# Optimization experiments

Measured on AMD Instinct MI355X. Metric: run time of the kernel, lower is better.

Reference implementation:

```python
import jax, jax.numpy as jnp
import numpy as np

B, T, D, H = 8, 2048, 1024, 1024

def setup_inputs() -> dict:
    key = jax.random.key(0)
    k1, k2, k3, k4 = jax.random.split(key, 4)
    scale = 1.0 / np.sqrt(D)
    return {
        "x": jax.random.normal(k1, (B, T, D), dtype=jnp.float32),
        "Wq": jax.random.normal(k2, (D, H), dtype=jnp.float32) * scale,
        "Wk": jax.random.normal(k3, (D, H), dtype=jnp.float32) * scale,
        "Wv": jax.random.normal(k4, (D, H), dtype=jnp.float32) * scale,
    }

def reference(x, Wq, Wk, Wv):
    # Single-head causal self-attention (dropout in eval mode = identity)
    q = jnp.einsum('btd,dh->bth', x, Wq)
    k = jnp.einsum('btd,dh->bth', x, Wk)
    v = jnp.einsum('btd,dh->bth', x, Wv)
    inv_sqrt_h = 1.0 / jnp.sqrt(jnp.asarray(q.shape[-1], q.dtype))
    scores = jnp.einsum('bqh,bkh->bqk', q, k) * inv_sqrt_h  # [B, T, T]
    Tq = scores.shape[-1]
    causal = jnp.tril(jnp.ones((Tq, Tq), dtype=bool))
    scores = jnp.where(causal, scores, jnp.asarray(-jnp.inf, scores.dtype))
    weights = jax.nn.softmax(scores, axis=-1)
    return jnp.einsum('bqk,bkh->bqh', weights, v)
```

## Files before the change

### kernel.cpp

```cpp
#include <hip/hip_runtime.h>

#define Bn 8
#define Tn 2048
#define Dn 1024
#define Hn 1024
#define Mn (Bn * Tn)

typedef __attribute__((ext_vector_type(8))) short bf16x8;
typedef __attribute__((ext_vector_type(4))) short short4v;
typedef __attribute__((ext_vector_type(16))) float f32x16;
typedef __attribute__((ext_vector_type(4))) float f32x4;

__device__ __forceinline__ unsigned short f2bf(float f) {
  union { float f; unsigned int u; } v; v.f = f;
  unsigned int u = v.u;
  u += 0x7FFFu + ((u >> 16) & 1u);
  return (unsigned short)(u >> 16);
}
__device__ __forceinline__ float bf2f(unsigned short h) {
  union { unsigned int u; float f; } v; v.u = ((unsigned int)h) << 16;
  return v.f;
}

__device__ __forceinline__ void gload_lds16(const unsigned short* g, unsigned short* l) {
  __builtin_amdgcn_global_load_lds((const __attribute__((address_space(1))) void*)g,
                                   (__attribute__((address_space(3))) void*)l, 16, 0, 0);
}


__device__ __forceinline__ void stage128x32s(const unsigned short* gbase, size_t row_stride,
                                             unsigned short* lds, int wave, int lane) {
#pragma unroll
  for (int c = 0; c < 2; ++c) {
    int rl = c * 16 + (lane >> 2);
    int pos = (lane & 3) ^ (rl & 3) ^ ((rl >> 2) & 3);
    const unsigned short* g = gbase + (size_t)(wave * 32 + rl) * row_stride + pos * 8;
    gload_lds16(g, lds + (wave * 32 + c * 16) * 32);
  }
}
__device__ __forceinline__ void stage128x64s(const unsigned short* gbase, size_t row_stride,
                                             unsigned short* lds0, unsigned short* lds1,
                                             int wave, int lane) {
  stage128x32s(gbase, row_stride, lds0, wave, lane);
  stage128x32s(gbase + 32, row_stride, lds1, wave, lane);
}

__device__ __forceinline__ void stage256x32s(const unsigned short* gbase, size_t row_stride,
                                             unsigned short* lds, int wave, int lane) {
#pragma unroll
  for (int c = 0; c < 2; ++c) {
    int rl = c * 16 + (lane >> 2);
    int pos = (lane & 3) ^ (rl & 3) ^ ((rl >> 2) & 3);
    const unsigned short* g = gbase + (size_t)(wave * 32 + rl) * row_stride + pos * 8;
    gload_lds16(g, lds + (wave * 32 + c * 16) * 32);
  }
}

__device__ __forceinline__ void mma_bk32(const unsigned short* lA, const unsigned short* lB,
                                         int wr, int wc, int l32, int half,
                                         f32x16 acc[2][2]) {
#pragma unroll
  for (int kk = 0; kk < 2; ++kk) {
    const int pos = (kk * 2 + half) ^ (l32 & 3) ^ ((l32 >> 2) & 3);
    bf16x8 af[2], bfr[2];
#pragma unroll
    for (int m = 0; m < 2; ++m)
      af[m] = *(const bf16x8*)&lA[(wr + m * 32 + l32) * 32 + pos * 8];
#pragma unroll
    for (int n = 0; n < 2; ++n)
      bfr[n] = *(const bf16x8*)&lB[(wc + n * 32 + l32) * 32 + pos * 8];
#pragma unroll
    for (int m = 0; m < 2; ++m)
#pragma unroll
      for (int n = 0; n < 2; ++n)
        acc[m][n] = __builtin_amdgcn_mfma_f32_32x32x16_bf16(af[m], bfr[n], acc[m][n], 0, 0, 0);
  }
}

__device__ __forceinline__ void rd4(const unsigned short* p, int rbase, int rl15, int csw,
                                    bf16x8 fr[4]) {
#pragma unroll
  for (int m = 0; m < 4; ++m)
    fr[m] = *(const bf16x8*)&p[(rbase + m * 16 + rl15) * 32 + csw * 8];
}

#define QKV_BAR  __builtin_amdgcn_s_barrier()
#define QKV_LGKM asm volatile("s_waitcnt lgkmcnt(0)" ::: "memory")
#define QKV_VM8  asm volatile("s_waitcnt vmcnt(8)" ::: "memory")
#define QKV_VM4  asm volatile("s_waitcnt vmcnt(4)" ::: "memory")
#define QKV_VM0  asm volatile("s_waitcnt vmcnt(0)" ::: "memory")

__global__ __launch_bounds__(256) void k_convert(const float* __restrict__ in,
                                                 unsigned short* __restrict__ out, int n4) {
  int idx = blockIdx.x * 256 + threadIdx.x;
  if (idx >= n4) return;
  float4 v = ((const float4*)in)[idx];
  short4v o;
  o.x = (short)f2bf(v.x); o.y = (short)f2bf(v.y);
  o.z = (short)f2bf(v.z); o.w = (short)f2bf(v.w);
  *(short4v*)(out + (size_t)idx * 4) = o;
}

__global__ __launch_bounds__(256) void k_cvt_w_t(const float* __restrict__ W0,
                                                 const float* __restrict__ W1,
                                                 const float* __restrict__ W2,
                                                 unsigned short* __restrict__ Wt3) {
  const int n0 = blockIdx.x * 64, k0 = blockIdx.y * 64, w = blockIdx.z;
  const float* W = (w == 0) ? W0 : (w == 1) ? W1 : W2;
  unsigned short* Wt = Wt3 + (size_t)w * Hn * Dn;
  __shared__ unsigned short lT[64 * 65];
  const int tid = threadIdx.x;
#pragma unroll
  for (int p = 0; p < 2; ++p) {
    int o = tid + p * 256;
    int r = o >> 3, c = (o & 7) * 8;
    const float* src = W + (size_t)(k0 + r) * Hn + n0 + c;
    float4 v0 = *(const float4*)src;
    float4 v1 = *(const float4*)(src + 4);
    unsigned short* d = &lT[r * 65 + c];
    d[0] = f2bf(v0.x); d[1] = f2bf(v0.y); d[2] = f2bf(v0.z); d[3] = f2bf(v0.w);
    d[4] = f2bf(v1.x); d[5] = f2bf(v1.y); d[6] = f2bf(v1.z); d[7] = f2bf(v1.w);
  }
  __syncthreads();
#pragma unroll
  for (int p = 0; p < 2; ++p) {
    int o = tid + p * 256;
    int r2 = o >> 3, c2 = (o & 7) * 8;
    bf16x8 v;
#pragma unroll
    for (int s = 0; s < 8; ++s) v[s] = (short)lT[(c2 + s) * 65 + r2];
    *(bf16x8*)(Wt + (size_t)(n0 + r2) * Dn + k0 + c2) = v;
  }
}

__global__ __launch_bounds__(512, 2) void gemm_qkv(const unsigned short* __restrict__ A,
                                                   const unsigned short* __restrict__ Wt3,
                                                   unsigned short* __restrict__ Q,
                                                   unsigned short* __restrict__ Kb,
                                                   unsigned short* __restrict__ Vt) {
  const int f = blockIdx.x;
  const int c = f & 7;
  const int q = f >> 3;
  const int nn = q % 12;
  const int w = nn >> 2;
  const int n0 = (nn & 3) * 256;
  const int m0 = ((q / 12) * 8 + c) * 256;
  const unsigned short* Bw = Wt3 + (size_t)w * Hn * Dn;
  __shared__ unsigned short lds[2][4][256 * 32];
  const int tid = threadIdx.x;
  const int lane = tid & 63, wave = tid >> 6;
  const int wr = (wave >> 2) * 128;
  const int wc = (wave & 3) * 64;
  const int rl15 = lane & 15, l4 = lane >> 4;
  const int csw = (l4 ^ (lane & 3) ^ ((lane >> 2) & 3)) & 3;

  f32x4 acc[8][4];
#pragma unroll
  for (int m = 0; m < 8; ++m)
#pragma unroll
    for (int n = 0; n < 4; ++n) acc[m][n] = (f32x4)(0.f);

  const unsigned short* Ab = A + (size_t)m0 * Dn;
  const unsigned short* Bb = Bw + (size_t)n0 * Dn;

  unsigned short* L0AL = &lds[0][0][0];
  unsigned short* L0AH = &lds[0][1][0];
  unsigned short* L0BL = &lds[0][2][0];
  unsigned short* L0BH = &lds[0][3][0];
  unsigned short* L1AL = &lds[1][0][0];
  unsigned short* L1AH = &lds[1][1][0];
  unsigned short* L1BL = &lds[1][2][0];
  unsigned short* L1BH = &lds[1][3][0];

  bf16x8 a0[4], a1[4], b0[4];
  auto RP = [&](const unsigned short* pa, const unsigned short* pb) {
    rd4(pa, wr, rl15, csw, a0);
    rd4(pa, wr + 64, rl15, csw, a1);
    rd4(pb, wc, rl15, csw, b0);
  };
  auto M32 = [&]() {
    __builtin_amdgcn_s_setprio(1);
#pragma unroll
    for (int m = 0; m < 4; ++m)
#pragma unroll
      for (int n = 0; n < 4; ++n)
        acc[m][n] = __builtin_amdgcn_mfma_f32_16x16x32_bf16(a0[m], b0[n], acc[m][n], 0, 0, 0);
#pragma unroll
    for (int m = 0; m < 4; ++m)
#pragma unroll
      for (int n = 0; n < 4; ++n)
        acc[m + 4][n] = __builtin_amdgcn_mfma_f32_16x16x32_bf16(a1[m], b0[n], acc[m + 4][n], 0, 0, 0);
    __builtin_amdgcn_s_setprio(0);
  };

  stage256x32s(Ab +  0, Dn, L0AL, wave, lane);
  stage256x32s(Bb +  0, Dn, L0BL, wave, lane);
  stage256x32s(Ab + 32, Dn, L0AH, wave, lane);
  stage256x32s(Bb + 32, Dn, L0BH, wave, lane);
  stage256x32s(Ab + 64, Dn, L1AL, wave, lane);
  stage256x32s(Bb + 64, Dn, L1BL, wave, lane);
  QKV_VM8;
  QKV_BAR;

#pragma unroll 1
  for (int i = 0; i < 6; ++i) {
    const int s1 = 2 * i + 1, s2 = 2 * i + 2, s3 = 2 * i + 3;
    RP(L0AL, L0BL);
    stage256x32s(Ab + s1 * 64 + 32, Dn, L1AH, wave, lane);
    stage256x32s(Bb + s1 * 64 + 32, Dn, L1BH, wave, lane);
    QKV_VM8; QKV_BAR; QKV_LGKM; M32(); QKV_BAR;
    RP(L0AH, L0BH);
    stage256x32s(Ab + s2 * 64, Dn, L0AL, wave, lane);
    stage256x32s(Bb + s2 * 64, Dn, L0BL, wave, lane);
    QKV_VM8; QKV_BAR; QKV_LGKM; M32(); QKV_BAR;
    RP(L1AL, L1BL);
    stage256x32s(Ab + s2 * 64 + 32, Dn, L0AH, wave, lane);
    stage256x32s(Bb + s2 * 64 + 32, Dn, L0BH, wave, lane);
    QKV_VM8; QKV_BAR; QKV_LGKM; M32(); QKV_BAR;
    RP(L1AH, L1BH);
    stage256x32s(Ab + s3 * 64, Dn, L1AL, wave, lane);
    stage256x32s(Bb + s3 * 64, Dn, L1BL, wave, lane);
    QKV_VM8; QKV_BAR; QKV_LGKM; M32(); QKV_BAR;
  }
  RP(L0AL, L0BL);
  stage256x32s(Ab + 13 * 64 + 32, Dn, L1AH, wave, lane);
  stage256x32s(Bb + 13 * 64 + 32, Dn, L1BH, wave, lane);
  QKV_VM8; QKV_BAR; QKV_LGKM; M32(); QKV_BAR;
  RP(L0AH, L0BH);
  stage256x32s(Ab + 14 * 64, Dn, L0AL, wave, lane);
  stage256x32s(Bb + 14 * 64, Dn, L0BL, wave, lane);
  QKV_VM8; QKV_BAR; QKV_LGKM; M32(); QKV_BAR;
  RP(L1AL, L1BL);
  stage256x32s(Ab + 14 * 64 + 32, Dn, L0AH, wave, lane);
  stage256x32s(Bb + 14 * 64 + 32, Dn, L0BH, wave, lane);
  QKV_VM8; QKV_BAR; QKV_LGKM; M32(); QKV_BAR;
  RP(L1AH, L1BH);
  stage256x32s(Ab + 15 * 64, Dn, L1AL, wave, lane);
  stage256x32s(Bb + 15 * 64, Dn, L1BL, wave, lane);
  QKV_VM8; QKV_BAR; QKV_LGKM; M32(); QKV_BAR;
  RP(L0AL, L0BL);
  stage256x32s(Ab + 15 * 64 + 32, Dn, L1AH, wave, lane);
  stage256x32s(Bb + 15 * 64 + 32, Dn, L1BH, wave, lane);
  QKV_VM8; QKV_BAR; QKV_LGKM; M32(); QKV_BAR;
  RP(L0AH, L0BH);
  QKV_VM4; QKV_BAR; QKV_LGKM; M32(); QKV_BAR;
  RP(L1AL, L1BL);
  QKV_VM0; QKV_BAR; QKV_LGKM; M32(); QKV_BAR;
  RP(L1AH, L1BH);
  QKV_LGKM; M32();

  if (w != 2) {
    unsigned short* Cp = (w == 0) ? Q : Kb;
#pragma unroll
    for (int m = 0; m < 8; ++m) {
      const int row = m0 + wr + m * 16 + l4 * 4;
#pragma unroll
      for (int n = 0; n < 4; ++n) {
        const int col = n0 + wc + n * 16 + rl15;
#pragma unroll
        for (int r = 0; r < 4; ++r)
          Cp[(size_t)(row + r) * Hn + col] = f2bf(acc[m][n][r]);
      }
    }
  } else {
    const int bb = m0 >> 11;
    const int tb = m0 & 2047;
#pragma unroll
    for (int m = 0; m < 8; ++m) {
      const int t0 = tb + wr + m * 16 + l4 * 4;
#pragma unroll
      for (int n = 0; n < 4; ++n) {
        const int h = n0 + wc + n * 16 + rl15;
        short4v o;
        o.x = (short)f2bf(acc[m][n][0]);
        o.y = (short)f2bf(acc[m][n][1]);
        o.z = (short)f2bf(acc[m][n][2]);
        o.w = (short)f2bf(acc[m][n][3]);
        *(short4v*)(Vt + ((size_t)bb * Hn + h) * Tn + t0) = o;
      }
    }
  }
}

__global__ __launch_bounds__(256) void gemm_scores(const unsigned short* __restrict__ Q,
                                                   const unsigned short* __restrict__ K,
                                                   unsigned short* __restrict__ S) {
  const int f = blockIdx.x;
  const int b = f & 7;
  const int q = f >> 3;
  const int rt = 15 - (q & 15);
  const int ct = q >> 4;
  if (ct > rt) return;
  const int j0 = ct * 128, i0 = rt * 128;
  const unsigned short* Qb = Q + (size_t)b * Tn * Hn;
  const unsigned short* Kp = K + (size_t)b * Tn * Hn;
  unsigned short* Sb = S + (size_t)b * Tn * Tn;
  __shared__ unsigned short lA[2][128 * 32];
  __shared__ unsigned short lB[2][128 * 32];
  const int tid = threadIdx.x;
  const int lane = tid & 63, wave = tid >> 6;
  const int wr = (wave >> 1) * 64, wc = (wave & 1) * 64;
  const int l32 = lane & 31, half = lane >> 5;

  f32x16 acc[2][2];
#pragma unroll
  for (int m = 0; m < 2; ++m)
#pragma unroll
    for (int n = 0; n < 2; ++n) acc[m][n] = (f32x16)(0.f);

  for (int kt = 0; kt < Hn / 64; ++kt) {
    stage128x64s(Qb + (size_t)i0 * Hn + kt * 64, Hn, lA[0], lA[1], wave, lane);
    stage128x64s(Kp + (size_t)j0 * Hn + kt * 64, Hn, lB[0], lB[1], wave, lane);
    __syncthreads();
    mma_bk32(lA[0], lB[0], wr, wc, l32, half, acc);
    mma_bk32(lA[1], lB[1], wr, wc, l32, half, acc);
    __syncthreads();
  }
#pragma unroll
  for (int m = 0; m < 2; ++m)
#pragma unroll
    for (int n = 0; n < 2; ++n) {
      int col = j0 + wc + n * 32 + l32;
#pragma unroll
      for (int qd = 0; qd < 4; ++qd) {
        int rb = i0 + wr + m * 32 + 8 * qd + 4 * half;
#pragma unroll
        for (int rr = 0; rr < 4; ++rr) {
          int row = rb + rr;
          float e = (col <= row) ? __expf(acc[m][n][qd * 4 + rr] * 0.03125f) : 0.f;
          Sb[(size_t)row * Tn + col] = f2bf(e);
        }
      }
    }
}

__global__ __launch_bounds__(256) void k_rowsum(const unsigned short* __restrict__ S,
                                                float* __restrict__ l) {
  const int b = blockIdx.y;
  const int i = blockIdx.x * 4 + (threadIdx.x >> 6);
  const int lane = threadIdx.x & 63;
  const unsigned short* row = S + ((size_t)b * Tn + i) * (size_t)Tn;
  const int npad = ((i >> 7) + 1) << 7;
  float s = 0.f;
  for (int j0 = 0; j0 < npad; j0 += 512) {
    int j = j0 + lane * 8;
    if (j < npad) {
      bf16x8 v = *(const bf16x8*)(row + j);
#pragma unroll
      for (int t = 0; t < 8; ++t) s += bf2f((unsigned short)v[t]);
    }
  }
#pragma unroll
  for (int off = 32; off > 0; off >>= 1) s += __shfl_down(s, off);
  if (lane == 0) l[(size_t)b * Tn + i] = s;
}

__global__ __launch_bounds__(256) void gemm_out(const unsigned short* __restrict__ P,
                                                const unsigned short* __restrict__ Vt,
                                                const float* __restrict__ lbuf,
                                                float* __restrict__ O) {
  const int f = blockIdx.x;
  const int b = f & 7;
  const int q = f >> 3;
  const int n0 = (q & 7) * 128;
  const int rt = 15 - (q >> 3);
  const int i0 = rt * 128;
  const int nkt = (rt + 1) * 2;
  const unsigned short* Pb = P + (size_t)b * Tn * Tn;
  const unsigned short* Vb = Vt + (size_t)b * Tn * Hn;
  __shared__ unsigned short lA[2][128 * 32];
  __shared__ unsigned short lB[2][128 * 32];
  const int tid = threadIdx.x;
  const int lane = tid & 63, wave = tid >> 6;
  const int wr = (wave >> 1) * 64, wc = (wave & 1) * 64;
  const int l32 = lane & 31, half = lane >> 5;

  f32x16 acc[2][2];
#pragma unroll
  for (int m = 0; m < 2; ++m)
#pragma unroll
    for (int n = 0; n < 2; ++n) acc[m][n] = (f32x16)(0.f);

  for (int kt = 0; kt < nkt; ++kt) {
    stage128x64s(Pb + (size_t)i0 * Tn + kt * 64, Tn, lA[0], lA[1], wave, lane);
    stage128x64s(Vb + (size_t)n0 * Tn + kt * 64, Tn, lB[0], lB[1], wave, lane);
    __syncthreads();
    mma_bk32(lA[0], lB[0], wr, wc, l32, half, acc);
    mma_bk32(lA[1], lB[1], wr, wc, l32, half, acc);
    __syncthreads();
  }
#pragma unroll
  for (int m = 0; m < 2; ++m)
#pragma unroll
    for (int n = 0; n < 2; ++n) {
      int col = n0 + wc + n * 32 + l32;
#pragma unroll
      for (int qd = 0; qd < 4; ++qd) {
        int rb = i0 + wr + m * 32 + 8 * qd + 4 * half;
        float4 lv = *(const float4*)&lbuf[(size_t)b * Tn + rb];
#pragma unroll
        for (int rr = 0; rr < 4; ++rr) {
          float inv = 1.f / ((&lv.x)[rr]);
          O[((size_t)b * Tn + rb + rr) * Hn + col] = acc[m][n][qd * 4 + rr] * inv;
        }
      }
    }
}

extern "C" void kernel_launch(void* const* d_in, const int* in_sizes, int n_in,
                              void* d_out, int out_size, void* d_ws, size_t ws_size,
                              hipStream_t stream) {
  const float* x  = (const float*)d_in[0];
  const float* Wq = (const float*)d_in[1];
  const float* Wk = (const float*)d_in[2];
  const float* Wv = (const float*)d_in[3];
  float* out = (float*)d_out;

  char* ws = (char*)d_ws;
  const size_t MiB = 1024 * 1024;
  unsigned short* Wt3 = (unsigned short*)(ws + 0 * MiB);
  unsigned short* xb  = (unsigned short*)(ws + 6 * MiB);
  unsigned short* Qb  = (unsigned short*)(ws + 38 * MiB);
  unsigned short* Kb  = (unsigned short*)(ws + 70 * MiB);
  unsigned short* Vt  = (unsigned short*)(ws + 102 * MiB);
  unsigned short* S   = (unsigned short*)(ws + 134 * MiB);
  float*          lrow = (float*)(ws + 6 * MiB);

  {
    int n4 = (Mn * Dn) / 4;
    k_convert<<<dim3(n4 / 256), 256, 0, stream>>>(x, xb, n4);
  }
  {
    dim3 g(Hn / 64, Dn / 64, 3);
    k_cvt_w_t<<<g, 256, 0, stream>>>(Wq, Wk, Wv, Wt3);
  }
  {
    gemm_qkv<<<dim3(768), 512, 0, stream>>>(xb, Wt3, Qb, Kb, Vt);
  }
  {
    gemm_scores<<<dim3(2048), 256, 0, stream>>>(Qb, Kb, S);
  }
  {
    k_rowsum<<<dim3(Tn / 4, Bn), 256, 0, stream>>>(S, lrow);
  }
  {
    gemm_out<<<dim3(1024), 256, 0, stream>>>(S, Vt, lrow, out);
  }
}
```

Before: 348.1 us.

## Pipeline attention GEMMs with 16x16 MFMA, triangular grid, fused rowsum via atomics

Rewrites the scores and output GEMMs to use a double-buffered LDS pipeline with 16x16x32 MFMA, async prefetch of the next k-slices, and raised wave priority around the MFMA blocks. The scores grid now covers only the 136 lower-triangular tiles per batch instead of launching 256 and exiting early. The row-sum kernel is removed: row sums are accumulated in the scores epilogue through shuffle reductions and atomicAdd into a buffer zeroed by a memset. This cuts a separate pass over S and one launch, at the cost of atomics and more registers per thread.

```diff
diff --git a/kernel.cpp b/kernel.cpp
--- a/kernel.cpp
+++ b/kernel.cpp
@@ -8,7 +8,6 @@
 
 typedef __attribute__((ext_vector_type(8))) short bf16x8;
 typedef __attribute__((ext_vector_type(4))) short short4v;
-typedef __attribute__((ext_vector_type(16))) float f32x16;
 typedef __attribute__((ext_vector_type(4))) float f32x4;
 
 __device__ __forceinline__ unsigned short f2bf(float f) {
@@ -38,12 +37,6 @@
     gload_lds16(g, lds + (wave * 32 + c * 16) * 32);
   }
 }
-__device__ __forceinline__ void stage128x64s(const unsigned short* gbase, size_t row_stride,
-                                             unsigned short* lds0, unsigned short* lds1,
-                                             int wave, int lane) {
-  stage128x32s(gbase, row_stride, lds0, wave, lane);
-  stage128x32s(gbase + 32, row_stride, lds1, wave, lane);
-}
 
 __device__ __forceinline__ void stage256x32s(const unsigned short* gbase, size_t row_stride,
                                              unsigned short* lds, int wave, int lane) {
@@ -53,27 +46,6 @@
     int pos = (lane & 3) ^ (rl & 3) ^ ((rl >> 2) & 3);
     const unsigned short* g = gbase + (size_t)(wave * 32 + rl) * row_stride + pos * 8;
     gload_lds16(g, lds + (wave * 32 + c * 16) * 32);
-  }
-}
-
-__device__ __forceinline__ void mma_bk32(const unsigned short* lA, const unsigned short* lB,
-                                         int wr, int wc, int l32, int half,
-                                         f32x16 acc[2][2]) {
-#pragma unroll
-  for (int kk = 0; kk < 2; ++kk) {
-    const int pos = (kk * 2 + half) ^ (l32 & 3) ^ ((l32 >> 2) & 3);
-    bf16x8 af[2], bfr[2];
-#pragma unroll
-    for (int m = 0; m < 2; ++m)
-      af[m] = *(const bf16x8*)&lA[(wr + m * 32 + l32) * 32 + pos * 8];
-#pragma unroll
-    for (int n = 0; n < 2; ++n)
-      bfr[n] = *(const bf16x8*)&lB[(wc + n * 32 + l32) * 32 + pos * 8];
-#pragma unroll
-    for (int m = 0; m < 2; ++m)
-#pragma unroll
-      for (int n = 0; n < 2; ++n)
-        acc[m][n] = __builtin_amdgcn_mfma_f32_32x32x16_bf16(af[m], bfr[n], acc[m][n], 0, 0, 0);
   }
 }
 
@@ -282,83 +254,112 @@
   }
 }
 
-__global__ __launch_bounds__(256) void gemm_scores(const unsigned short* __restrict__ Q,
-                                                   const unsigned short* __restrict__ K,
-                                                   unsigned short* __restrict__ S) {
+__global__ __launch_bounds__(256, 2) void gemm_scores(const unsigned short* __restrict__ Q,
+                                                      const unsigned short* __restrict__ K,
+                                                      unsigned short* __restrict__ S,
+                                                      float* __restrict__ lrow) {
   const int f = blockIdx.x;
   const int b = f & 7;
-  const int q = f >> 3;
-  const int rt = 15 - (q & 15);
-  const int ct = q >> 4;
-  if (ct > rt) return;
-  const int j0 = ct * 128, i0 = rt * 128;
-  const unsigned short* Qb = Q + (size_t)b * Tn * Hn;
-  const unsigned short* Kp = K + (size_t)b * Tn * Hn;
+  const int u = f >> 3;
+  int rt = (int)((sqrtf(8.f * (float)u + 1.f) - 1.f) * 0.5f);
+  if ((rt + 1) * (rt + 2) / 2 <= u) ++rt;
+  if (rt * (rt + 1) / 2 > u) --rt;
+  const int ct = u - rt * (rt + 1) / 2;
+  const int i0 = rt * 128, j0 = ct * 128;
+  const unsigned short* Ag = Q + (size_t)b * Tn * Hn + (size_t)i0 * Hn;
+  const unsigned short* Bg = K + (size_t)b * Tn * Hn + (size_t)j0 * Hn;
   unsigned short* Sb = S + (size_t)b * Tn * Tn;
-  __shared__ unsigned short lA[2][128 * 32];
-  __shared__ unsigned short lB[2][128 * 32];
+  __shared__ unsigned short lds[2][4][128 * 32];
   const int tid = threadIdx.x;
   const int lane = tid & 63, wave = tid >> 6;
   const int wr = (wave >> 1) * 64, wc = (wave & 1) * 64;
-  const int l32 = lane & 31, half = lane >> 5;
-
-  f32x16 acc[2][2];
-#pragma unroll
-  for (int m = 0; m < 2; ++m)
-#pragma unroll
-    for (int n = 0; n < 2; ++n) acc[m][n] = (f32x16)(0.f);
-
-  for (int kt = 0; kt < Hn / 64; ++kt) {
-    stage128x64s(Qb + (size_t)i0 * Hn + kt * 64, Hn, lA[0], lA[1], wave, lane);
-    stage128x64s(Kp + (size_t)j0 * Hn + kt * 64, Hn, lB[0], lB[1], wave, lane);
-    __syncthreads();
-    mma_bk32(lA[0], lB[0], wr, wc, l32, half, acc);
-    mma_bk32(lA[1], lB[1], wr, wc, l32, half, acc);
-    __syncthreads();
-  }
-#pragma unroll
-  for (int m = 0; m < 2; ++m)
-#pragma unroll
-    for (int n = 0; n < 2; ++n) {
-      int col = j0 + wc + n * 32 + l32;
-#pragma unroll
-      for (int qd = 0; qd < 4; ++qd) {
-        int rb = i0 + wr + m * 32 + 8 * qd + 4 * half;
-#pragma unroll
-        for (int rr = 0; rr < 4; ++rr) {
-          int row = rb + rr;
-          float e = (col <= row) ? __expf(acc[m][n][qd * 4 + rr] * 0.03125f) : 0.f;
-          Sb[(size_t)row * Tn + col] = f2bf(e);
-        }
+  const int rl15 = lane & 15, l4 = lane >> 4;
+  const int csw = (l4 ^ (lane & 3) ^ ((lane >> 2) & 3)) & 3;
+
+  f32x4 acc[4][4];
+#pragma unroll
+  for (int m = 0; m < 4; ++m)
+#pragma unroll
+    for (int n = 0; n < 4; ++n) acc[m][n] = (f32x4)(0.f);
+
+  bf16x8 a0[4], b0[4];
+  auto M16 = [&]() {
+    __builtin_amdgcn_s_setprio(1);
+#pragma unroll
+    for (int m = 0; m < 4; ++m)
+#pragma unroll
+      for (int n = 0; n < 4; ++n)
+        acc[m][n] = __builtin_amdgcn_mfma_f32_16x16x32_bf16(a0[m], b0[n], acc[m][n], 0, 0, 0);
+    __builtin_amdgcn_s_setprio(0);
+  };
+
+  const int nkt = Hn / 64;
+  stage128x32s(Ag +  0, Hn, &lds[0][0][0], wave, lane);
+  stage128x32s(Bg +  0, Hn, &lds[0][2][0], wave, lane);
+  stage128x32s(Ag + 32, Hn, &lds[0][1][0], wave, lane);
+  stage128x32s(Bg + 32, Hn, &lds[0][3][0], wave, lane);
+  stage128x32s(Ag + 64, Hn, &lds[1][0][0], wave, lane);
+  stage128x32s(Bg + 64, Hn, &lds[1][2][0], wave, lane);
+  QKV_VM8; QKV_BAR;
+
+#pragma unroll 1
+  for (int t = 0; t < nkt; ++t) {
+    const int cb = t & 1, nb = cb ^ 1;
+    rd4(&lds[cb][0][0], wr, rl15, csw, a0);
+    rd4(&lds[cb][2][0], wc, rl15, csw, b0);
+    {
+      const int ts = (t + 1 < nkt) ? t + 1 : nkt - 1;
+      stage128x32s(Ag + ts * 64 + 32, Hn, &lds[nb][1][0], wave, lane);
+      stage128x32s(Bg + ts * 64 + 32, Hn, &lds[nb][3][0], wave, lane);
+    }
+    QKV_VM8; QKV_BAR; QKV_LGKM; M16(); QKV_BAR;
+    rd4(&lds[cb][1][0], wr, rl15, csw, a0);
+    rd4(&lds[cb][3][0], wc, rl15, csw, b0);
+    {
+      const int ts = (t + 2 < nkt) ? t + 2 : nkt - 1;
+      stage128x32s(Ag + ts * 64, Hn, &lds[cb][0][0], wave, lane);
+      stage128x32s(Bg + ts * 64, Hn, &lds[cb][2][0], wave, lane);
+    }
+    QKV_VM8; QKV_BAR; QKV_LGKM; M16(); QKV_BAR;
+  }
+  QKV_VM0;
+
+  float rs[4][4];
+#pragma unroll
+  for (int m = 0; m < 4; ++m)
+#pragma unroll
+    for (int r = 0; r < 4; ++r) rs[m][r] = 0.f;
+#pragma unroll
+  for (int m = 0; m < 4; ++m) {
+    const int row = i0 + wr + m * 16 + l4 * 4;
+#pragma unroll
+    for (int n = 0; n < 4; ++n) {
+      const int col = j0 + wc + n * 16 + rl15;
+#pragma unroll
+      for (int r = 0; r < 4; ++r) {
+        float e = (col <= row + r) ? __expf(acc[m][n][r] * 0.03125f) : 0.f;
+        unsigned short eb = f2bf(e);
+        Sb[(size_t)(row + r) * Tn + col] = eb;
+        rs[m][r] += bf2f(eb);
       }
     }
-}
-
-__global__ __launch_bounds__(256) void k_rowsum(const unsigned short* __restrict__ S,
-                                                float* __restrict__ l) {
-  const int b = blockIdx.y;
-  const int i = blockIdx.x * 4 + (threadIdx.x >> 6);
-  const int lane = threadIdx.x & 63;
-  const unsigned short* row = S + ((size_t)b * Tn + i) * (size_t)Tn;
-  const int npad = ((i >> 7) + 1) << 7;
-  float s = 0.f;
-  for (int j0 = 0; j0 < npad; j0 += 512) {
-    int j = j0 + lane * 8;
-    if (j < npad) {
-      bf16x8 v = *(const bf16x8*)(row + j);
-#pragma unroll
-      for (int t = 0; t < 8; ++t) s += bf2f((unsigned short)v[t]);
-    }
-  }
-#pragma unroll
-  for (int off = 32; off > 0; off >>= 1) s += __shfl_down(s, off);
-  if (lane == 0) l[(size_t)b * Tn + i] = s;
-}
-
-__global__ __launch_bounds__(256) void gemm_out(const unsigned short* __restrict__ P,
-                                                const unsigned short* __restrict__ Vt,
-                                                const float* __restrict__ lbuf,
-                                                float* __restrict__ O) {
+  }
+#pragma unroll
+  for (int m = 0; m < 4; ++m)
+#pragma unroll
+    for (int r = 0; r < 4; ++r) {
+#pragma unroll
+      for (int msk = 1; msk < 16; msk <<= 1)
+        rs[m][r] += __shfl_xor(rs[m][r], msk);
+      if (rl15 == 0)
+        atomicAdd(&lrow[(size_t)b * Tn + i0 + wr + m * 16 + l4 * 4 + r], rs[m][r]);
+    }
+}
+
+__global__ __launch_bounds__(256, 2) void gemm_out(const unsigned short* __restrict__ P,
+                                                   const unsigned short* __restrict__ Vt,
+                                                   const float* __restrict__ lbuf,
+                                                   float* __restrict__ O) {
   const int f = blockIdx.x;
   const int b = f & 7;
   const int q = f >> 3;
@@ -366,45 +367,76 @@
   const int rt = 15 - (q >> 3);
   const int i0 = rt * 128;
   const int nkt = (rt + 1) * 2;
-  const unsigned short* Pb = P + (size_t)b * Tn * Tn;
-  const unsigned short* Vb = Vt + (size_t)b * Tn * Hn;
-  __shared__ unsigned short lA[2][128 * 32];
-  __shared__ unsigned short lB[2][128 * 32];
+  const unsigned short* Ag = P + (size_t)b * Tn * Tn + (size_t)i0 * Tn;
+  const unsigned short* Bg = Vt + (size_t)b * Tn * Hn + (size_t)n0 * Tn;
+  __shared__ unsigned short lds[2][4][128 * 32];
   const int tid = threadIdx.x;
   const int lane = tid & 63, wave = tid >> 6;
   const int wr = (wave >> 1) * 64, wc = (wave & 1) * 64;
-  const int l32 = lane & 31, half = lane >> 5;
-
-  f32x16 acc[2][2];
-#pragma unroll
-  for (int m = 0; m < 2; ++m)
-#pragma unroll
-    for (int n = 0; n < 2; ++n) acc[m][n] = (f32x16)(0.f);
-
-  for (int kt = 0; kt < nkt; ++kt) {
-    stage128x64s(Pb + (size_t)i0 * Tn + kt * 64, Tn, lA[0], lA[1], wave, lane);
-    stage128x64s(Vb + (size_t)n0 * Tn + kt * 64, Tn, lB[0], lB[1], wave, lane);
-    __syncthreads();
-    mma_bk32(lA[0], lB[0], wr, wc, l32, half, acc);
-    mma_bk32(lA[1], lB[1], wr, wc, l32, half, acc);
-    __syncthreads();
-  }
-#pragma unroll
-  for (int m = 0; m < 2; ++m)
-#pragma unroll
-    for (int n = 0; n < 2; ++n) {
-      int col = n0 + wc + n * 32 + l32;
-#pragma unroll
-      for (int qd = 0; qd < 4; ++qd) {
-        int rb = i0 + wr + m * 32 + 8 * qd + 4 * half;
-        float4 lv = *(const float4*)&lbuf[(size_t)b * Tn + rb];
-#pragma unroll
-        for (int rr = 0; rr < 4; ++rr) {
-          float inv = 1.f / ((&lv.x)[rr]);
-          O[((size_t)b * Tn + rb + rr) * Hn + col] = acc[m][n][qd * 4 + rr] * inv;
-        }
-      }
-    }
+  const int rl15 = lane & 15, l4 = lane >> 4;
+  const int csw = (l4 ^ (lane & 3) ^ ((lane >> 2) & 3)) & 3;
+
+  f32x4 acc[4][4];
+#pragma unroll
+  for (int m = 0; m < 4; ++m)
+#pragma unroll
+    for (int n = 0; n < 4; ++n) acc[m][n] = (f32x4)(0.f);
+
+  bf16x8 a0[4], b0[4];
+  auto M16 = [&]() {
+    __builtin_amdgcn_s_setprio(1);
+#pragma unroll
+    for (int m = 0; m < 4; ++m)
+#pragma unroll
+      for (int n = 0; n < 4; ++n)
+        acc[m][n] = __builtin_amdgcn_mfma_f32_16x16x32_bf16(a0[m], b0[n], acc[m][n], 0, 0, 0);
+    __builtin_amdgcn_s_setprio(0);
+  };
+
+  stage128x32s(Ag +  0, Tn, &lds[0][0][0], wave, lane);
+  stage128x32s(Bg +  0, Tn, &lds[0][2][0], wave, lane);
+  stage128x32s(Ag + 32, Tn, &lds[0][1][0], wave, lane);
+  stage128x32s(Bg + 32, Tn, &lds[0][3][0], wave, lane);
+  stage128x32s(Ag + 64, Tn, &lds[1][0][0], wave, lane);
+  stage128x32s(Bg + 64, Tn, &lds[1][2][0], wave, lane);
+  QKV_VM8; QKV_BAR;
+
+#pragma unroll 1
+  for (int t = 0; t < nkt; ++t) {
+    const int cb = t & 1, nb = cb ^ 1;
+    rd4(&lds[cb][0][0], wr, rl15, csw, a0);
+    rd4(&lds[cb][2][0], wc, rl15, csw, b0);
+    {
+      const int ts = (t + 1 < nkt) ? t + 1 : nkt - 1;
+      stage128x32s(Ag + ts * 64 + 32, Tn, &lds[nb][1][0], wave, lane);
+      stage128x32s(Bg + ts * 64 + 32, Tn, &lds[nb][3][0], wave, lane);
+    }
+    QKV_VM8; QKV_BAR; QKV_LGKM; M16(); QKV_BAR;
+    rd4(&lds[cb][1][0], wr, rl15, csw, a0);
+    rd4(&lds[cb][3][0], wc, rl15, csw, b0);
+    {
+      const int ts = (t + 2 < nkt) ? t + 2 : nkt - 1;
+      stage128x32s(Ag + ts * 64, Tn, &lds[cb][0][0], wave, lane);
+      stage128x32s(Bg + ts * 64, Tn, &lds[cb][2][0], wave, lane);
+    }
+    QKV_VM8; QKV_BAR; QKV_LGKM; M16(); QKV_BAR;
+  }
+  QKV_VM0;
+
+#pragma unroll
+  for (int m = 0; m < 4; ++m) {
+    const int rb = i0 + wr + m * 16 + l4 * 4;
+    float4 lv = *(const float4*)&lbuf[(size_t)b * Tn + rb];
+    const float inv0 = 1.f / lv.x, inv1 = 1.f / lv.y, inv2 = 1.f / lv.z, inv3 = 1.f / lv.w;
+#pragma unroll
+    for (int n = 0; n < 4; ++n) {
+      const int col = n0 + wc + n * 16 + rl15;
+      O[((size_t)b * Tn + rb + 0) * Hn + col] = acc[m][n][0] * inv0;
+      O[((size_t)b * Tn + rb + 1) * Hn + col] = acc[m][n][1] * inv1;
+      O[((size_t)b * Tn + rb + 2) * Hn + col] = acc[m][n][2] * inv2;
+      O[((size_t)b * Tn + rb + 3) * Hn + col] = acc[m][n][3] * inv3;
+    }
+  }
 }
 
 extern "C" void kernel_launch(void* const* d_in, const int* in_sizes, int n_in,
@@ -437,11 +469,9 @@
   {
     gemm_qkv<<<dim3(768), 512, 0, stream>>>(xb, Wt3, Qb, Kb, Vt);
   }
+  hipMemsetAsync(lrow, 0, (size_t)Bn * Tn * sizeof(float), stream);
   {
-    gemm_scores<<<dim3(2048), 256, 0, stream>>>(Qb, Kb, S);
-  }
-  {
-    k_rowsum<<<dim3(Tn / 4, Bn), 256, 0, stream>>>(S, lrow);
+    gemm_scores<<<dim3(1088), 256, 0, stream>>>(Qb, Kb, S, lrow);
   }
   {
     gemm_out<<<dim3(1024), 256, 0, stream>>>(S, Vt, lrow, out);
```

After: 350.4 us. About the same (+0.7%).
